# Optimization experiments

Hardware: AMD Instinct MI355X
Metric: run time of the kernel (lower is better)

Reference implementation:

```python
import jax, jax.numpy as jnp
import numpy as np

B, T, N, D = 32, 336, 321, 3
G = 512          # global_hidden
L = 2            # layer_nums
E = 4            # experts per layer
K = 2            # top-k
F = 2048         # d_ff (expert hidden)
P = 96           # pred_len
LOSS_COEF = 0.01


def setup_inputs() -> dict:
    key = jax.random.key(0)
    ks = iter(jax.random.split(key, 24))
    rn = lambda shape, s=0.02: jax.random.normal(next(ks), shape, jnp.float32) * s
    return {
        "x": jax.random.normal(next(ks), (B, T, N, D), jnp.float32),
        # GlobalEmbedding
        "Wv": rn((N, 1)), "bv": jnp.zeros((1,), jnp.float32),
        "Wt": rn((T, G)), "bt": jnp.zeros((G,), jnp.float32),
        # CrossAttention
        "Wq": rn((G, G)), "bq": jnp.zeros((G,), jnp.float32),
        "Wk": rn((G, G)), "bk": jnp.zeros((G,), jnp.float32),
        "Wva": rn((G, G)), "bva": jnp.zeros((G,), jnp.float32),
        # AMS MoE layers (stacked over L)
        "Wg": rn((L, T, E)),
        "We1": rn((L, E, T, F)), "be1": jnp.zeros((L, E, F), jnp.float32),
        "We2": rn((L, E, F, T)), "be2": jnp.zeros((L, E, T), jnp.float32),
        # projections head
        "P1w": rn((T, P)), "P1b": jnp.zeros((P,), jnp.float32),
        "P2w": rn((P, 2 * P)), "P2b": jnp.zeros((2 * P,), jnp.float32),
    }


def _cv_squared(v):
    return v.var() / (v.mean() ** 2 + 1e-10)


def reference(x, Wv, bv, Wt, bt, Wq, bq, Wk, bk, Wva, bva,
              Wg, We1, be1, We2, be2, P1w, P1b, P2w, P2b):
    Bv, Tv, Nv, Dv = x.shape
    # ---- GlobalEmbedding: (B,T,N,D) -> (B,D,G), with the original's raw reshape
    g = jnp.einsum('btvd,vo->btdo', x, Wv)[..., 0] + bv[0]        # (B,T,D)
    g2 = g.reshape(Bv * Dv, Tv) @ Wt + bt                          # faithful contiguous reshape
    gf = g2.reshape(Bv, Dv, -1)                                    # (B,D,G)
    # ---- CrossAttention (no sqrt(d) scaling, per source)
    q = gf @ Wq + bq
    kk = gf @ Wk + bk
    v = gf @ Wva + bva
    attn = jax.nn.softmax(jnp.einsum('big,bjg->bij', q, kk), axis=-1)
    sst_attended = jnp.einsum('bij,bjg->big', attn, v)[:, 0, :]    # unused: use_attend=0
    del sst_attended
    # ---- slice value channel + RevIN norm over time
    x0 = x[..., 0]                                                 # (B,T,N)
    mu = x0.mean(axis=1, keepdims=True)
    sd = jnp.sqrt(x0.var(axis=1, keepdims=True) + 1e-5)
    out = (x0 - mu) / sd
    # ---- AMS layers: clean top-k gated MoE over per-node seq MLP experts
    balance_loss = jnp.float32(0.0)
    for l in range(L):
        logits = out.mean(axis=2) @ Wg[l]                          # (B,E)
        topv, topi = jax.lax.top_k(logits, K)
        gates = jnp.zeros_like(logits).at[
            jnp.arange(Bv)[:, None], topi].set(jax.nn.softmax(topv, axis=-1))
        importance = gates.sum(axis=0)
        balance_loss = balance_loss + _cv_squared(importance) * LOSS_COEF
        xt = out.transpose(0, 2, 1)                                # (B,N,T)
        h = jax.nn.relu(jnp.einsum('bnt,etf->ebnf', xt, We1[l])
                        + be1[l][:, None, None, :])                # (E,B,N,F)
        eo = jnp.einsum('ebnf,eft->ebnt', h, We2[l]) + be2[l][:, None, None, :]
        moe = jnp.einsum('be,ebnt->bnt', gates, eo).transpose(0, 2, 1)
        out = out + moe                                            # residual_connection=1
    # ---- projection head
    o = out.transpose(0, 2, 1)                                     # (B,N,T)
    hproj = jnp.tanh(o @ P1w + P1b)
    p = (hproj @ P2w + P2b).reshape(Bv, Nv, P, 2).transpose(0, 2, 1, 3)  # (B,P,N,2)
    mean = p[..., 0]
    std = jax.nn.softplus(p[..., 1]) + 1e-6
    return mean, balance_loss, std
```

## Files before the change

### kernel.cpp

```cpp
#include <hip/hip_runtime.h>
#include <hip/hip_bf16.h>
#include <cstdint>
#include <math.h>

#define B_ 32
#define T_ 336
#define N_ 321
#define L_ 2
#define E_ 4
#define F_ 2048
#define P_ 96
#define TPAD 352
#define NPAD 384

typedef __hip_bfloat16 bf16;
typedef __attribute__((ext_vector_type(8))) __bf16 bf16x8;
typedef __attribute__((ext_vector_type(4))) float f32x4;


__device__ __forceinline__ void async_copy16(const void* g, void* l) {
  __builtin_amdgcn_global_load_lds(
      (__attribute__((address_space(1))) void*)(uintptr_t)g,
      (__attribute__((address_space(3))) void*)(unsigned int)(uintptr_t)l,
      16, 0, 0);
}

__global__ void transpose_cast_kernel(const float* __restrict__ src, bf16* __restrict__ dst,
                                      int R, int C, int Rp, int Cp,
                                      long long sStride, long long dStride) {
  __shared__ float tile[32][33];
  const float* s = src + (size_t)blockIdx.z * sStride;
  bf16* d = dst + (size_t)blockIdx.z * dStride;
  int r0 = blockIdx.x * 32, c0 = blockIdx.y * 32;
  int tx = threadIdx.x, ty = threadIdx.y;
  #pragma unroll
  for (int ii = 0; ii < 4; ii++) {
    int rl = ty * 4 + ii;
    int r = r0 + rl, c = c0 + tx;
    tile[rl][tx] = (r < R && c < C) ? s[(size_t)r * C + c] : 0.f;
  }
  __syncthreads();
  #pragma unroll
  for (int ii = 0; ii < 4; ii++) {
    int cl = ty * 4 + ii;
    int cd = c0 + cl, rd = r0 + tx;
    if (cd < Cp && rd < Rp)
      d[(size_t)cd * Rp + rd] = __float2bfloat16(tile[tx][cl]);
  }
}

__global__ void repack_w2_kernel(const float* __restrict__ src, bf16* __restrict__ dst) {
  __shared__ float tile[32][96];
  int le = blockIdx.z, tb = blockIdx.y, f0 = blockIdx.x * 32;
  int tid = threadIdx.x;
  const float* s = src + (size_t)le * F_ * T_;
  for (int idx = tid; idx < 32 * 96; idx += 256) {
    int ff = idx / 96, tt = idx % 96;
    int t = tb * 96 + tt;
    tile[ff][tt] = (t < T_) ? s[(size_t)(f0 + ff) * T_ + t] : 0.f;
  }
  __syncthreads();
  bf16* d = dst + ((size_t)le * 4 + tb) * 196608 + (size_t)(f0 >> 3) * 768;
  for (int s2 = tid; s2 < 384; s2 += 256) {
    int kgl = s2 / 96, row = s2 % 96;
    bf16 v[8];
    #pragma unroll
    for (int j = 0; j < 8; j++) v[j] = __float2bfloat16(tile[kgl * 8 + j][row]);
    *(uint4*)(d + (size_t)kgl * 768 + row * 8) = *(const uint4*)v;
  }
}

__global__ void revin_kernel(const float* __restrict__ x, float* __restrict__ out,
                             bf16* __restrict__ Abuf) {
  int b = blockIdx.x;
  int n = blockIdx.y * 128 + threadIdx.x;
  if (n >= NPAD) return;
  bf16* arow = Abuf + ((size_t)b * NPAD + n) * TPAD;
  if (n >= N_) {
    for (int t = 0; t < TPAD; t++) arow[t] = __float2bfloat16(0.f);
    return;
  }
  const float* xp = x + ((size_t)b * T_ * N_ + n) * 3;
  float s1 = 0.f, s2 = 0.f;
  for (int t = 0; t < T_; t++) {
    float v = xp[(size_t)t * N_ * 3];
    s1 += v; s2 += v * v;
  }
  float mu = s1 / T_;
  float var = s2 / T_ - mu * mu;
  float inv = 1.f / sqrtf(var + 1e-5f);
  for (int t = 0; t < T_; t++) {
    float v = (xp[(size_t)t * N_ * 3] - mu) * inv;
    out[((size_t)b * T_ + t) * N_ + n] = v;
    arow[t] = __float2bfloat16(v);
  }
  for (int t = T_; t < TPAD; t++) arow[t] = __float2bfloat16(0.f);
}

__global__ void gate1_kernel(const float* __restrict__ out, float* __restrict__ colsum) {
  int b = blockIdx.y;
  int w = threadIdx.x >> 6, lane = threadIdx.x & 63;
  int t = blockIdx.x * 16 + w * 4;
  #pragma unroll
  for (int i = 0; i < 4; i++, t++) {
    const float* p = out + ((size_t)b * T_ + t) * N_;
    float s = 0.f;
    for (int n = lane; n < N_; n += 64) s += p[n];
    #pragma unroll
    for (int off = 32; off; off >>= 1) s += __shfl_down(s, off);
    if (lane == 0) colsum[b * T_ + t] = s;
  }
}

__global__ void gate2_kernel(const float* __restrict__ colsum, const float* __restrict__ Wg,
                             int* __restrict__ pair_e, float* __restrict__ pair_gate,
                             float* __restrict__ loss_partial, int layer) {
  __shared__ float lg[32][4];
  __shared__ float gates[32][4];
  __shared__ float imp[4];
  int tid = threadIdx.x;
  if (tid < 128) {
    int b = tid >> 2, e = tid & 3;
    float s = 0.f;
    for (int t = 0; t < T_; t++)
      s += colsum[b * T_ + t] * Wg[(layer * T_ + t) * E_ + e];
    lg[b][e] = s / (float)N_;
  }
  __syncthreads();
  if (tid < 32) {
    float v[4];
    #pragma unroll
    for (int e = 0; e < 4; e++) v[e] = lg[tid][e];
    int i0 = 0;
    for (int e = 1; e < 4; e++) if (v[e] > v[i0]) i0 = e;
    int i1 = -1;
    for (int e = 0; e < 4; e++) {
      if (e == i0) continue;
      if (i1 < 0 || v[e] > v[i1]) i1 = e;
    }
    float ex = expf(v[i1] - v[i0]);
    float g0 = 1.f / (1.f + ex);
    float g1 = ex / (1.f + ex);
    pair_e[tid * 2] = i0; pair_e[tid * 2 + 1] = i1;
    pair_gate[tid * 2] = g0; pair_gate[tid * 2 + 1] = g1;
    #pragma unroll
    for (int e = 0; e < 4; e++) gates[tid][e] = 0.f;
    gates[tid][i0] = g0; gates[tid][i1] = g1;
  }
  __syncthreads();
  if (tid < 4) {
    float s = 0.f;
    for (int bb = 0; bb < 32; bb++) s += gates[bb][tid];
    imp[tid] = s;
  }
  __syncthreads();
  if (tid == 0) {
    float m = (imp[0] + imp[1] + imp[2] + imp[3]) * 0.25f;
    float va = 0.f;
    #pragma unroll
    for (int e = 0; e < 4; e++) { float d = imp[e] - m; va += d * d; }
    va *= 0.25f;
    loss_partial[layer] = 0.01f * (va / (m * m + 1e-10f));
  }
}

__global__ __launch_bounds__(256) void gemm1_kernel(
    const bf16* __restrict__ Abuf, const bf16* __restrict__ W1T,
    const float* __restrict__ be1, const int* __restrict__ pair_e,
    const float* __restrict__ pair_gate, bf16* __restrict__ h, int layer) {
  __shared__ __align__(16) bf16 As[128 * 32];
  __shared__ __align__(16) bf16 Bs[128 * 32];
  __shared__ float bias_s[128];

  const int tid = threadIdx.x;
  const int w = tid >> 6, lane = tid & 63;
  const int pair = blockIdx.z;
  const int b = pair >> 1;
  const int e = pair_e[pair];
  const float gate = pair_gate[pair];
  const int m0 = blockIdx.y * 128;
  const int f0 = blockIdx.x * 128;

  const bf16* Ag = Abuf + (size_t)b * NPAD * TPAD + (size_t)m0 * TPAD;
  const bf16* Bg = W1T + ((size_t)(layer * E_ + e) * F_ + f0) * TPAD;
  if (tid < 128) bias_s[tid] = be1[(size_t)(layer * E_ + e) * F_ + f0 + tid];

  f32x4 acc[4][4];
  const f32x4 zero = {0.f, 0.f, 0.f, 0.f};
  #pragma unroll
  for (int i = 0; i < 4; i++)
    #pragma unroll
    for (int j = 0; j < 4; j++) acc[i][j] = zero;

  const int wm = w >> 1, wn = w & 1;
  const int lrow = lane >> 2;
  const int lkoff = (lane & 3) * 8;
  const int quad = lane >> 4;
  const int l15 = lane & 15;

  for (int kk = 0; kk < TPAD / 32; ++kk) {
    const int k0 = kk * 32;
    #pragma unroll
    for (int i = 0; i < 2; i++) {
      int r = (w * 2 + i) * 16 + lrow;
      async_copy16(Ag + (size_t)r * TPAD + k0 + lkoff, As + (w * 2 + i) * 512);
    }
    #pragma unroll
    for (int i = 0; i < 2; i++) {
      int r = (w * 2 + i) * 16 + lrow;
      async_copy16(Bg + (size_t)r * TPAD + k0 + lkoff, Bs + (w * 2 + i) * 512);
    }
    __syncthreads();
    bf16x8 af[4], bfr[4];
    #pragma unroll
    for (int mi = 0; mi < 4; mi++)
      af[mi] = *(const bf16x8*)(As + (wm * 64 + mi * 16 + l15) * 32 + quad * 8);
    #pragma unroll
    for (int ni = 0; ni < 4; ni++)
      bfr[ni] = *(const bf16x8*)(Bs + (wn * 64 + ni * 16 + l15) * 32 + quad * 8);
    #pragma unroll
    for (int mi = 0; mi < 4; mi++)
      #pragma unroll
      for (int ni = 0; ni < 4; ni++)
        acc[mi][ni] = __builtin_amdgcn_mfma_f32_16x16x32_bf16(af[mi], bfr[ni], acc[mi][ni], 0, 0, 0);
    __syncthreads();
  }

  bf16* tw0 = As + w * 1024;
  bf16* tw1 = Bs + w * 1024;
  size_t hb = (size_t)pair * 786432 + (size_t)((m0 >> 6) + wm) * 131072;
  const int kgbase = (f0 >> 3) + wn * 8 + (lane & 3) * 2;
  #pragma unroll
  for (int mi = 0; mi < 4; mi++) {
    bf16* tw = (mi & 1) ? tw1 : tw0;
    #pragma unroll
    for (int ni = 0; ni < 4; ni++) {
      float bias = bias_s[wn * 64 + ni * 16 + l15];
      #pragma unroll
      for (int r = 0; r < 4; r++) {
        float v = acc[mi][ni][r] + bias;
        v = fmaxf(v, 0.f) * gate;
        tw[(quad * 4 + r) * 64 + ni * 16 + l15] = __float2bfloat16(v);
      }
    }
    int row = lane >> 2;
    int fpart = (lane & 3) * 16;
    const uint4* sp = (const uint4*)(tw + row * 64 + fpart);
    uint4 d0 = sp[0];
    uint4 d1 = sp[1];
    bf16* dp = h + hb + (size_t)kgbase * 512 + (mi * 16 + row) * 8;
    *(uint4*)dp = d0;
    *(uint4*)(dp + 512) = d1;
  }
}

#define CT_STRIDE 104
__global__ __launch_bounds__(256) void gemm2_kernel(
    const bf16* __restrict__ h, const bf16* __restrict__ W2B,
    const float* __restrict__ be2, const int* __restrict__ pair_e,
    const float* __restrict__ pair_gate, float* __restrict__ out,
    bf16* __restrict__ Abuf, int layer) {
  __shared__ __align__(16) bf16 S[10240];
  __shared__ float bias_t[96];
  bf16* As2 = S;
  bf16* Bs2 = S + 4096;

  const int tid = threadIdx.x;
  const int w = tid >> 6, lane = tid & 63;
  const int id = blockIdx.x;
  const int u = id & 7;
  const int v = id >> 3;
  const int tt = v & 3;
  const int pn = u + 8 * (v >> 2);
  const int b = pn / 6, nt = pn % 6;
  const int n0 = nt * 64, t0 = tt * 96;

  const int e0 = pair_e[b * 2], e1 = pair_e[b * 2 + 1];
  const float g0 = pair_gate[b * 2], g1 = pair_gate[b * 2 + 1];
  const bf16* Agb0 = h + ((size_t)(b * 2) * 6 + nt) * 131072;
  const bf16* Agb1 = h + ((size_t)(b * 2 + 1) * 6 + nt) * 131072;
  const bf16* Bgb0 = W2B + ((size_t)(layer * E_ + e0) * 4 + tt) * 196608;
  const bf16* Bgb1 = W2B + ((size_t)(layer * E_ + e1) * 4 + tt) * 196608;
  const int quad = lane >> 4, l15 = lane & 15;
  const int wm = w >> 1, wt = w & 1;

  if (tid < 96) {
    int t = t0 + tid;
    bias_t[tid] = (t < T_)
        ? g0 * be2[(layer * E_ + e0) * T_ + t] + g1 * be2[(layer * E_ + e1) * T_ + t]
        : 0.f;
  }

  f32x4 acc[2][3];
  const f32x4 zero = {0.f, 0.f, 0.f, 0.f};
  #pragma unroll
  for (int i = 0; i < 2; i++)
    #pragma unroll
    for (int jj = 0; jj < 3; jj++) acc[i][jj] = zero;

  for (int kk = 0; kk < 64; ++kk) {
    const bf16* Aj = ((kk < 32) ? Agb0 : Agb1) + (size_t)(kk & 31) * 4096;
    const bf16* Bj = ((kk < 32) ? Bgb0 : Bgb1) + (size_t)(kk & 31) * 6144;
    #pragma unroll
    for (int i = 0; i < 2; i++)
      async_copy16(Aj + (w * 2 + i) * 512 + lane * 8, As2 + (w * 2 + i) * 512);
    #pragma unroll
    for (int i = 0; i < 3; i++)
      async_copy16(Bj + (w * 3 + i) * 512 + lane * 8, Bs2 + (w * 3 + i) * 512);
    __syncthreads();
    #pragma unroll
    for (int w32 = 0; w32 < 2; w32++) {
      const int kg = w32 * 4 + quad;
      bf16x8 af[2], bfr[3];
      #pragma unroll
      for (int mi = 0; mi < 2; mi++)
        af[mi] = *(const bf16x8*)(As2 + kg * 512 + (wm * 32 + mi * 16 + l15) * 8);
      #pragma unroll
      for (int ni = 0; ni < 3; ni++)
        bfr[ni] = *(const bf16x8*)(Bs2 + kg * 768 + (wt * 48 + ni * 16 + l15) * 8);
      #pragma unroll
      for (int mi = 0; mi < 2; mi++)
        #pragma unroll
        for (int ni = 0; ni < 3; ni++)
          acc[mi][ni] = __builtin_amdgcn_mfma_f32_16x16x32_bf16(af[mi], bfr[ni], acc[mi][ni], 0, 0, 0);
    }
    __syncthreads();
  }

  #pragma unroll
  for (int mi = 0; mi < 2; mi++) {
    #pragma unroll
    for (int ni = 0; ni < 3; ni++) {
      int nloc_b = wm * 32 + mi * 16 + quad * 4;
      int tloc = wt * 48 + ni * 16 + l15;
      int t = t0 + tloc;
      #pragma unroll
      for (int r = 0; r < 4; r++) {
        int nloc = nloc_b + r;
        int n = n0 + nloc;
        float vv = 0.f;
        if (n < N_ && t < T_) {
          size_t q = ((size_t)b * T_ + t) * N_ + n;
          vv = out[q] + acc[mi][ni][r] + bias_t[tloc];
          out[q] = vv;
        }
        S[nloc * CT_STRIDE + tloc] = __float2bfloat16(vv);
      }
    }
  }
  __syncthreads();
  #pragma unroll
  for (int it = 0; it < 3; ++it) {
    int idx = tid + it * 256;
    int row = idx / 12, seg = idx % 12;
    int t = t0 + seg * 8;
    if (t < TPAD)
      *(uint4*)(Abuf + ((size_t)b * NPAD + n0 + row) * TPAD + t) =
          *(const uint4*)(S + row * CT_STRIDE + seg * 8);
  }
}

#define HS_STRIDE 104
__global__ __launch_bounds__(256) void proj_kernel(
    const bf16* __restrict__ Abuf, const bf16* __restrict__ P1T, const float* __restrict__ P1b,
    const bf16* __restrict__ P2T, const float* __restrict__ P2b,
    const float* __restrict__ loss_partial, float* __restrict__ dout) {
  __shared__ __align__(16) bf16 Hs[128 * HS_STRIDE];
  const int tid = threadIdx.x;
  const int w = tid >> 6, lane = tid & 63;
  const int quad = lane >> 4, l15 = lane & 15;
  const int b = blockIdx.y;
  const int m0 = blockIdx.x * 128;

  f32x4 acc1[2][6];
  const f32x4 zero = {0.f, 0.f, 0.f, 0.f};
  #pragma unroll
  for (int i = 0; i < 2; i++)
    #pragma unroll
    for (int j = 0; j < 6; j++) acc1[i][j] = zero;

  const bf16* Arow = Abuf + ((size_t)b * NPAD + m0 + w * 32) * TPAD;
  for (int kk = 0; kk < TPAD / 32; ++kk) {
    bf16x8 af[2], bfr[6];
    #pragma unroll
    for (int mi = 0; mi < 2; mi++)
      af[mi] = *(const bf16x8*)(Arow + (size_t)(mi * 16 + l15) * TPAD + kk * 32 + quad * 8);
    #pragma unroll
    for (int ni = 0; ni < 6; ni++)
      bfr[ni] = *(const bf16x8*)(P1T + (size_t)(ni * 16 + l15) * TPAD + kk * 32 + quad * 8);
    #pragma unroll
    for (int mi = 0; mi < 2; mi++)
      #pragma unroll
      for (int ni = 0; ni < 6; ni++)
        acc1[mi][ni] = __builtin_amdgcn_mfma_f32_16x16x32_bf16(af[mi], bfr[ni], acc1[mi][ni], 0, 0, 0);
  }

  #pragma unroll
  for (int mi = 0; mi < 2; mi++) {
    #pragma unroll
    for (int ni = 0; ni < 6; ni++) {
      float bias = P1b[ni * 16 + l15];
      #pragma unroll
      for (int r = 0; r < 4; r++) {
        float x = acc1[mi][ni][r] + bias;
        float t = 1.f - 2.f / (__expf(2.f * x) + 1.f);
        Hs[(w * 32 + mi * 16 + quad * 4 + r) * HS_STRIDE + ni * 16 + l15] = __float2bfloat16(t);
      }
    }
  }
  __syncthreads();

  #pragma unroll
  for (int half = 0; half < 2; ++half) {
    f32x4 acc2[2][6];
    #pragma unroll
    for (int i = 0; i < 2; i++)
      #pragma unroll
      for (int j = 0; j < 6; j++) acc2[i][j] = zero;

    #pragma unroll
    for (int kk = 0; kk < 3; ++kk) {
      bf16x8 af[2], bfr[6];
      #pragma unroll
      for (int mi = 0; mi < 2; mi++)
        af[mi] = *(const bf16x8*)(Hs + (w * 32 + mi * 16 + l15) * HS_STRIDE + kk * 32 + quad * 8);
      #pragma unroll
      for (int ni = 0; ni < 6; ni++)
        bfr[ni] = *(const bf16x8*)(P2T + (size_t)((half * 6 + ni) * 16 + l15) * P_ + kk * 32 + quad * 8);
      #pragma unroll
      for (int mi = 0; mi < 2; mi++)
        #pragma unroll
        for (int ni = 0; ni < 6; ni++)
          acc2[mi][ni] = __builtin_amdgcn_mfma_f32_16x16x32_bf16(af[mi], bfr[ni], acc2[mi][ni], 0, 0, 0);
    }

    #pragma unroll
    for (int mi = 0; mi < 2; mi++) {
      #pragma unroll
      for (int ni = 0; ni < 6; ni++) {
        int jj = (half * 6 + ni) * 16 + l15;
        float bias = P2b[jj];
        int pout = jj >> 1;
        #pragma unroll
        for (int r = 0; r < 4; r++) {
          int n = m0 + w * 32 + mi * 16 + quad * 4 + r;
          if (n < N_) {
            float s = acc2[mi][ni][r] + bias;
            size_t o = ((size_t)b * P_ + pout) * N_ + n;
            if ((jj & 1) == 0) {
              dout[o] = s;
            } else {
              float sp = (s > 20.f) ? s : log1pf(__expf(s));
              dout[(size_t)B_ * P_ * N_ + 1 + o] = sp + 1e-6f;
            }
          }
        }
      }
    }
  }
  if (b == 0 && blockIdx.x == 0 && tid == 0)
    dout[(size_t)B_ * P_ * N_] = loss_partial[0] + loss_partial[1];
}

extern "C" void kernel_launch(void* const* d_in, const int* in_sizes, int n_in,
                              void* d_out, int out_size, void* d_ws, size_t ws_size,
                              hipStream_t stream) {
  const float* x   = (const float*)d_in[0];
  const float* Wg  = (const float*)d_in[11];
  const float* We1 = (const float*)d_in[12];
  const float* be1 = (const float*)d_in[13];
  const float* We2 = (const float*)d_in[14];
  const float* be2 = (const float*)d_in[15];
  const float* P1w = (const float*)d_in[16];
  const float* P1b = (const float*)d_in[17];
  const float* P2w = (const float*)d_in[18];
  const float* P2b = (const float*)d_in[19];

  char* ws = (char*)d_ws;
  size_t off = 0;
  auto alloc = [&](size_t bytes) -> void* {
    void* p = ws + off;
    off += (bytes + 255) & ~(size_t)255;
    return p;
  };
  float* out        = (float*)alloc((size_t)B_ * T_ * N_ * 4);
  bf16*  Abuf       = (bf16*) alloc((size_t)B_ * NPAD * TPAD * 2);
  bf16*  W1T        = (bf16*) alloc((size_t)L_ * E_ * F_ * TPAD * 2);
  bf16*  W2B        = (bf16*) alloc((size_t)L_ * E_ * 4 * 196608 * 2);
  bf16*  P1T        = (bf16*) alloc((size_t)P_ * TPAD * 2);
  bf16*  P2T        = (bf16*) alloc((size_t)2 * P_ * P_ * 2);
  bf16*  h          = (bf16*) alloc((size_t)B_ * 2 * 786432 * 2);
  float* colsum     = (float*)alloc((size_t)B_ * T_ * 4);
  int*   pair_e     = (int*)  alloc(B_ * 2 * 4);
  float* pair_gate  = (float*)alloc(B_ * 2 * 4);
  float* loss_part  = (float*)alloc(2 * 4);
  if (ws_size < off) return;

  dim3 tb(32, 8);
  transpose_cast_kernel<<<dim3(11, 64, 8), tb, 0, stream>>>(
      We1, W1T, T_, F_, TPAD, F_, (long long)T_ * F_, (long long)F_ * TPAD);
  repack_w2_kernel<<<dim3(64, 4, 8), 256, 0, stream>>>(We2, W2B);
  transpose_cast_kernel<<<dim3(11, 3, 1), tb, 0, stream>>>(
      P1w, P1T, T_, P_, TPAD, P_, 0, 0);
  transpose_cast_kernel<<<dim3(3, 6, 1), tb, 0, stream>>>(
      P2w, P2T, P_, 2 * P_, P_, 2 * P_, 0, 0);

  revin_kernel<<<dim3(B_, 3), 128, 0, stream>>>(x, out, Abuf);

  for (int l = 0; l < L_; ++l) {
    gate1_kernel<<<dim3(21, B_), 256, 0, stream>>>(out, colsum);
    gate2_kernel<<<1, 128, 0, stream>>>(colsum, Wg, pair_e, pair_gate, loss_part, l);
    gemm1_kernel<<<dim3(16, 3, 64), 256, 0, stream>>>(Abuf, W1T, be1, pair_e, pair_gate, h, l);
    gemm2_kernel<<<768, 256, 0, stream>>>(h, W2B, be2, pair_e, pair_gate, out, Abuf, l);
  }

  proj_kernel<<<dim3(3, B_), 256, 0, stream>>>(Abuf, P1T, P1b, P2T, P2b, loss_part,
                                               (float*)d_out);
}
```

Baseline: 596.5 us.

## Double-buffer gemm2 A tiles in LDS and load B fragments straight to registers

Rewrites the gemm2 main loop as a two-stage software pipeline. A tiles are double-buffered in LDS with async copies issued one step ahead. B fragments now go directly from global memory into registers, ping-ponging between two register sets instead of being staged through LDS. This removes one barrier per iteration and overlaps loads with MFMA work, at the cost of more registers and uncoalesced-looking direct B loads.

New measurement: 612.9 us. 1.03x slower.

```diff
diff --git a/kernel.cpp b/kernel.cpp
--- a/kernel.cpp
+++ b/kernel.cpp
@@ -255,15 +255,52 @@
 }
 
 #define CT_STRIDE 104
+
+#define G2_STEP(KK, BC, BN)                                                     \
+  {                                                                             \
+    const int kkn = (KK) + 1;                                                   \
+    if (kkn < 64) {                                                             \
+      const bf16* Aj = ((kkn < 32) ? Agb0 : Agb1) + (size_t)(kkn & 31) * 4096;  \
+      bf16* An = S + ((kkn & 1) << 12);                                         \
+      async_copy16(Aj + aoff, An + w * 1024);                                   \
+      async_copy16(Aj + aoff + 512, An + w * 1024 + 512);                       \
+      const bf16* Bj = ((kkn < 32) ? Bgb0 : Bgb1) + (size_t)(kkn & 31) * 6144;  \
+      _Pragma("unroll")                                                         \
+      for (int w32 = 0; w32 < 2; w32++)                                         \
+        _Pragma("unroll")                                                       \
+        for (int ni = 0; ni < 3; ni++)                                          \
+          BN[w32][ni] = *(const bf16x8*)(Bj + boff + w32 * 3072 + ni * 128);    \
+    }                                                                           \
+    const bf16* Ac = S + (((KK) & 1) << 12);                                    \
+    bf16x8 af0[2], af1[2];                                                      \
+    _Pragma("unroll")                                                           \
+    for (int mi = 0; mi < 2; mi++)                                              \
+      af0[mi] = *(const bf16x8*)(Ac + afoff + mi * 128);                        \
+    _Pragma("unroll")                                                           \
+    for (int mi = 0; mi < 2; mi++)                                              \
+      af1[mi] = *(const bf16x8*)(Ac + afoff + 2048 + mi * 128);                 \
+    _Pragma("unroll")                                                           \
+    for (int mi = 0; mi < 2; mi++)                                              \
+      _Pragma("unroll")                                                         \
+      for (int ni = 0; ni < 3; ni++)                                            \
+        acc[mi][ni] = __builtin_amdgcn_mfma_f32_16x16x32_bf16(                  \
+            af0[mi], BC[0][ni], acc[mi][ni], 0, 0, 0);                          \
+    _Pragma("unroll")                                                           \
+    for (int mi = 0; mi < 2; mi++)                                              \
+      _Pragma("unroll")                                                         \
+      for (int ni = 0; ni < 3; ni++)                                            \
+        acc[mi][ni] = __builtin_amdgcn_mfma_f32_16x16x32_bf16(                  \
+            af1[mi], BC[1][ni], acc[mi][ni], 0, 0, 0);                          \
+    __syncthreads();                                                            \
+  }
+
 __global__ __launch_bounds__(256) void gemm2_kernel(
     const bf16* __restrict__ h, const bf16* __restrict__ W2B,
     const float* __restrict__ be2, const int* __restrict__ pair_e,
     const float* __restrict__ pair_gate, float* __restrict__ out,
     bf16* __restrict__ Abuf, int layer) {
-  __shared__ __align__(16) bf16 S[10240];
+  __shared__ __align__(16) bf16 S[8192];
   __shared__ float bias_t[96];
-  bf16* As2 = S;
-  bf16* Bs2 = S + 4096;
 
   const int tid = threadIdx.x;
   const int w = tid >> 6, lane = tid & 63;
@@ -298,33 +335,23 @@
     #pragma unroll
     for (int jj = 0; jj < 3; jj++) acc[i][jj] = zero;
 
-  for (int kk = 0; kk < 64; ++kk) {
-    const bf16* Aj = ((kk < 32) ? Agb0 : Agb1) + (size_t)(kk & 31) * 4096;
-    const bf16* Bj = ((kk < 32) ? Bgb0 : Bgb1) + (size_t)(kk & 31) * 6144;
-    #pragma unroll
-    for (int i = 0; i < 2; i++)
-      async_copy16(Aj + (w * 2 + i) * 512 + lane * 8, As2 + (w * 2 + i) * 512);
-    #pragma unroll
-    for (int i = 0; i < 3; i++)
-      async_copy16(Bj + (w * 3 + i) * 512 + lane * 8, Bs2 + (w * 3 + i) * 512);
-    __syncthreads();
-    #pragma unroll
-    for (int w32 = 0; w32 < 2; w32++) {
-      const int kg = w32 * 4 + quad;
-      bf16x8 af[2], bfr[3];
-      #pragma unroll
-      for (int mi = 0; mi < 2; mi++)
-        af[mi] = *(const bf16x8*)(As2 + kg * 512 + (wm * 32 + mi * 16 + l15) * 8);
-      #pragma unroll
-      for (int ni = 0; ni < 3; ni++)
-        bfr[ni] = *(const bf16x8*)(Bs2 + kg * 768 + (wt * 48 + ni * 16 + l15) * 8);
-      #pragma unroll
-      for (int mi = 0; mi < 2; mi++)
-        #pragma unroll
-        for (int ni = 0; ni < 3; ni++)
-          acc[mi][ni] = __builtin_amdgcn_mfma_f32_16x16x32_bf16(af[mi], bfr[ni], acc[mi][ni], 0, 0, 0);
-    }
-    __syncthreads();
+  const int aoff = w * 1024 + lane * 8;
+  const int boff = quad * 768 + (wt * 48 + l15) * 8;
+  const int afoff = quad * 512 + (wm * 32 + l15) * 8;
+
+  async_copy16(Agb0 + aoff, S + w * 1024);
+  async_copy16(Agb0 + aoff + 512, S + w * 1024 + 512);
+  bf16x8 bA[2][3], bB[2][3];
+  #pragma unroll
+  for (int w32 = 0; w32 < 2; w32++)
+    #pragma unroll
+    for (int ni = 0; ni < 3; ni++)
+      bA[w32][ni] = *(const bf16x8*)(Bgb0 + boff + w32 * 3072 + ni * 128);
+  __syncthreads();
+
+  for (int kk2 = 0; kk2 < 32; ++kk2) {
+    G2_STEP(2 * kk2, bA, bB);
+    G2_STEP(2 * kk2 + 1, bB, bA);
   }
 
   #pragma unroll
```

## Double-buffer LDS tiles in both expert GEMM kernels to overlap loads with MFMA

Applied to the files above, without the earlier changes.

Both expert GEMM kernels now use two LDS buffers. The async global-to-LDS copy for the next K-slice is issued before the MFMAs on the current slice, so only one barrier per iteration remains. That barrier is a custom one that waits on vmcnt and then calls s_barrier, meant to hide global load latency behind matrix math. The cost is double the LDS footprint per block, which may lower occupancy. The hand-written waitcnt and barrier sequence also has to be exactly right to avoid read-after-write races.

Measured after the change: 584.3 us. 1.02x faster.

```diff
diff --git a/kernel.cpp b/kernel.cpp
--- a/kernel.cpp
+++ b/kernel.cpp
@@ -23,6 +23,18 @@
       (__attribute__((address_space(1))) void*)(uintptr_t)g,
       (__attribute__((address_space(3))) void*)(unsigned int)(uintptr_t)l,
       16, 0, 0);
+}
+
+__device__ __forceinline__ void pipe_barrier_vm0() {
+  asm volatile("s_waitcnt vmcnt(0)" ::: "memory");
+  __builtin_amdgcn_s_barrier();
+  __builtin_amdgcn_sched_barrier(0);
+}
+
+__device__ __forceinline__ void pipe_barrier_full() {
+  asm volatile("s_waitcnt vmcnt(0) lgkmcnt(0)" ::: "memory");
+  __builtin_amdgcn_s_barrier();
+  __builtin_amdgcn_sched_barrier(0);
 }
 
 __global__ void transpose_cast_kernel(const float* __restrict__ src, bf16* __restrict__ dst,
@@ -168,8 +180,7 @@
     const bf16* __restrict__ Abuf, const bf16* __restrict__ W1T,
     const float* __restrict__ be1, const int* __restrict__ pair_e,
     const float* __restrict__ pair_gate, bf16* __restrict__ h, int layer) {
-  __shared__ __align__(16) bf16 As[128 * 32];
-  __shared__ __align__(16) bf16 Bs[128 * 32];
+  __shared__ __align__(16) bf16 S1[16384];
   __shared__ float bias_s[128];
 
   const int tid = threadIdx.x;
@@ -198,19 +209,25 @@
   const int quad = lane >> 4;
   const int l15 = lane & 15;
 
-  for (int kk = 0; kk < TPAD / 32; ++kk) {
-    const int k0 = kk * 32;
+  auto stage1 = [&](int k, int buf) {
+    const int k0 = k * 32;
+    bf16* As = S1 + buf * 8192;
+    bf16* Bs = As + 4096;
     #pragma unroll
     for (int i = 0; i < 2; i++) {
       int r = (w * 2 + i) * 16 + lrow;
       async_copy16(Ag + (size_t)r * TPAD + k0 + lkoff, As + (w * 2 + i) * 512);
-    }
-    #pragma unroll
-    for (int i = 0; i < 2; i++) {
-      int r = (w * 2 + i) * 16 + lrow;
       async_copy16(Bg + (size_t)r * TPAD + k0 + lkoff, Bs + (w * 2 + i) * 512);
     }
-    __syncthreads();
+  };
+
+  stage1(0, 0);
+  pipe_barrier_full();
+
+  for (int kk = 0; kk < TPAD / 32; ++kk) {
+    if (kk < TPAD / 32 - 1) stage1(kk + 1, (kk + 1) & 1);
+    const bf16* As = S1 + (kk & 1) * 8192;
+    const bf16* Bs = As + 4096;
     bf16x8 af[4], bfr[4];
     #pragma unroll
     for (int mi = 0; mi < 4; mi++)
@@ -223,11 +240,11 @@
       #pragma unroll
       for (int ni = 0; ni < 4; ni++)
         acc[mi][ni] = __builtin_amdgcn_mfma_f32_16x16x32_bf16(af[mi], bfr[ni], acc[mi][ni], 0, 0, 0);
-    __syncthreads();
-  }
-
-  bf16* tw0 = As + w * 1024;
-  bf16* tw1 = Bs + w * 1024;
+    pipe_barrier_vm0();
+  }
+
+  bf16* tw0 = S1 + w * 1024;
+  bf16* tw1 = S1 + 4096 + w * 1024;
   size_t hb = (size_t)pair * 786432 + (size_t)((m0 >> 6) + wm) * 131072;
   const int kgbase = (f0 >> 3) + wn * 8 + (lane & 3) * 2;
   #pragma unroll
@@ -260,10 +277,8 @@
     const float* __restrict__ be2, const int* __restrict__ pair_e,
     const float* __restrict__ pair_gate, float* __restrict__ out,
     bf16* __restrict__ Abuf, int layer) {
-  __shared__ __align__(16) bf16 S[10240];
+  __shared__ __align__(16) bf16 S[20480];
   __shared__ float bias_t[96];
-  bf16* As2 = S;
-  bf16* Bs2 = S + 4096;
 
   const int tid = threadIdx.x;
   const int w = tid >> 6, lane = tid & 63;
@@ -298,16 +313,26 @@
     #pragma unroll
     for (int jj = 0; jj < 3; jj++) acc[i][jj] = zero;
 
-  for (int kk = 0; kk < 64; ++kk) {
-    const bf16* Aj = ((kk < 32) ? Agb0 : Agb1) + (size_t)(kk & 31) * 4096;
-    const bf16* Bj = ((kk < 32) ? Bgb0 : Bgb1) + (size_t)(kk & 31) * 6144;
+  auto stage2 = [&](int k, int buf) {
+    const bf16* Aj = ((k < 32) ? Agb0 : Agb1) + (size_t)(k & 31) * 4096;
+    const bf16* Bj = ((k < 32) ? Bgb0 : Bgb1) + (size_t)(k & 31) * 6144;
+    bf16* As2 = S + buf * 10240;
+    bf16* Bs2 = As2 + 4096;
     #pragma unroll
     for (int i = 0; i < 2; i++)
       async_copy16(Aj + (w * 2 + i) * 512 + lane * 8, As2 + (w * 2 + i) * 512);
     #pragma unroll
     for (int i = 0; i < 3; i++)
       async_copy16(Bj + (w * 3 + i) * 512 + lane * 8, Bs2 + (w * 3 + i) * 512);
-    __syncthreads();
+  };
+
+  stage2(0, 0);
+  pipe_barrier_full();
+
+  for (int kk = 0; kk < 64; ++kk) {
+    if (kk < 63) stage2(kk + 1, (kk + 1) & 1);
+    const bf16* As2 = S + (kk & 1) * 10240;
+    const bf16* Bs2 = As2 + 4096;
     #pragma unroll
     for (int w32 = 0; w32 < 2; w32++) {
       const int kg = w32 * 4 + quad;
@@ -324,7 +349,7 @@
         for (int ni = 0; ni < 3; ni++)
           acc[mi][ni] = __builtin_amdgcn_mfma_f32_16x16x32_bf16(af[mi], bfr[ni], acc[mi][ni], 0, 0, 0);
     }
-    __syncthreads();
+    pipe_barrier_vm0();
   }
 
   #pragma unroll
```
